# Optimization experiments

Hardware: AMD Instinct MI355X
Metric: run time of the kernel (lower is better)

## Reference

```python
import jax, jax.numpy as jnp
import numpy as np

HIDDEN = 2048
NUM_HEAD = 32
GROUP = 8
HEAD_DIM = HIDDEN // NUM_HEAD  # 64
REP = NUM_HEAD // GROUP        # 4


def setup_inputs() -> dict:
    key = jax.random.key(0)
    ks = jax.random.split(key, 9)
    s = 0.02
    kv_dim = GROUP * HEAD_DIM
    return {
        "hidden_states": jax.random.normal(ks[0], (2, 2048, HIDDEN), dtype=jnp.float32),
        "Wq": jax.random.normal(ks[1], (HIDDEN, HIDDEN), dtype=jnp.float32) * s,
        "bq": jnp.zeros((HIDDEN,), dtype=jnp.float32),
        "Wk": jax.random.normal(ks[2], (HIDDEN, kv_dim), dtype=jnp.float32) * s,
        "bk": jnp.zeros((kv_dim,), dtype=jnp.float32),
        "Wv": jax.random.normal(ks[3], (HIDDEN, kv_dim), dtype=jnp.float32) * s,
        "bv": jnp.zeros((kv_dim,), dtype=jnp.float32),
        "Wo": jax.random.normal(ks[4], (HIDDEN, HIDDEN), dtype=jnp.float32) * s,
        "bo": jnp.zeros((HIDDEN,), dtype=jnp.float32),
    }


def reference(hidden_states, Wq, bq, Wk, bk, Wv, bv, Wo, bo):
    B, S, H = hidden_states.shape
    q = hidden_states @ Wq + bq                      # [B,S,H]
    k = hidden_states @ Wk + bk                      # [B,S,G*hd]
    v = hidden_states @ Wv + bv
    q = q.reshape(B, S, NUM_HEAD, HEAD_DIM).transpose(0, 2, 1, 3)   # [B,nh,S,hd]
    k = k.reshape(B, S, GROUP, HEAD_DIM).transpose(0, 2, 1, 3)      # [B,G,S,hd]
    v = v.reshape(B, S, GROUP, HEAD_DIM).transpose(0, 2, 1, 3)
    # expand KV heads: each group head repeated REP times contiguously
    k = jnp.repeat(k, REP, axis=1)                   # [B,nh,S,hd]
    v = jnp.repeat(v, REP, axis=1)
    scale = 1.0 / jnp.sqrt(jnp.float32(HEAD_DIM))
    scores = jnp.einsum("bhqd,bhkd->bhqk", q, k) * scale  # [B,nh,S,S]
    attn = jax.nn.softmax(scores, axis=-1)
    out = jnp.einsum("bhqk,bhkd->bhqd", attn, v)     # [B,nh,S,hd]
    out = out.transpose(0, 2, 1, 3).reshape(B, S, NUM_HEAD * HEAD_DIM)
    return out @ Wo + bo
```

## Files before the change

kernel.cpp:

```cpp
#include <hip/hip_runtime.h>
#include <hip/hip_bf16.h>

typedef __attribute__((ext_vector_type(8))) short bf16x8;
typedef __attribute__((ext_vector_type(4))) short bf16x4;
typedef __attribute__((ext_vector_type(4))) float f32x4;

__device__ __forceinline__ unsigned short f2bf(float f) {
  union { float f; unsigned int u; } v; v.f = f;
  unsigned int r = (v.u + 0x7fffu + ((v.u >> 16) & 1u)) >> 16;
  return (unsigned short)r;
}

__device__ __forceinline__ unsigned int pk2bf(float a, float b) {
  float2 t; t.x = a; t.y = b;
  __hip_bfloat162 h = __float22bfloat162_rn(t);
  union { __hip_bfloat162 h; unsigned int u; } cv; cv.h = h;
  return cv.u;
}

__device__ __forceinline__ void g2l16(unsigned short* lds, const unsigned short* g) {
  __builtin_amdgcn_global_load_lds(
      (const __attribute__((address_space(1))) unsigned int*)g,
      (__attribute__((address_space(3))) unsigned int*)lds, 16, 0, 0);
}


__global__ __launch_bounds__(256) void cast_hs_kernel(const float* __restrict__ in,
                                                      unsigned short* __restrict__ out) {
  size_t i = (size_t)blockIdx.x * 256 + threadIdx.x;
  float4 v = ((const float4*)in)[i];
  ushort4 o;
  o.x = f2bf(v.x); o.y = f2bf(v.y); o.z = f2bf(v.z); o.w = f2bf(v.w);
  ((ushort4*)out)[i] = o;
}

__global__ __launch_bounds__(256) void transpose_all_kernel(
    const float* __restrict__ Wq, const float* __restrict__ Wk,
    const float* __restrict__ Wv, const float* __restrict__ Wo,
    unsigned short* __restrict__ Wqkv, unsigned short* __restrict__ WoT) {
  __shared__ float tile[32][33];
  int z = blockIdx.z;
  const float* src; unsigned short* dst; int N;
  if (z == 0)      { src = Wq; dst = Wqkv;                          N = 2048; }
  else if (z == 1) { src = Wk; dst = Wqkv + (size_t)2048 * 2048;    N = 512; }
  else if (z == 2) { src = Wv; dst = Wqkv + (size_t)2560 * 2048;    N = 512; }
  else             { src = Wo; dst = WoT;                           N = 2048; }
  if (blockIdx.x * 32 >= N) return;
  int n0 = blockIdx.x * 32, k0 = blockIdx.y * 32;
  int t = threadIdx.x;
  for (int i = 0; i < 4; ++i) {
    int linear = i * 256 + t;
    int kr = linear >> 5, nc = linear & 31;
    tile[kr][nc] = src[(size_t)(k0 + kr) * N + (n0 + nc)];
  }
  __syncthreads();
  for (int i = 0; i < 4; ++i) {
    int linear = i * 256 + t;
    int nr = linear >> 5, kc = linear & 31;
    dst[(size_t)(n0 + nr) * 2048 + (k0 + kc)] = f2bf(tile[kc][nr]);
  }
}


#define QSCALE 0.18033688011112042f

__global__ __launch_bounds__(256) void gemm_qkv_kernel(
    const unsigned short* __restrict__ A, const unsigned short* __restrict__ Bt,
    const float* __restrict__ bq, const float* __restrict__ bk, const float* __restrict__ bv,
    unsigned short* __restrict__ Qb, unsigned short* __restrict__ Kb,
    unsigned short* __restrict__ Vtb) {
  __shared__ __align__(16) unsigned short smem[128 * 136];
  unsigned short* sA = smem;
  unsigned short* sB = smem + 4096;
  const int K = 2048;
  int bm0 = blockIdx.y * 128, bn0 = blockIdx.x * 128;
  int t = threadIdx.x;
  int w = t >> 6, lane = t & 63, l16 = lane & 15, quad = lane >> 4;
  int wm = (w & 1) * 64, wn = (w >> 1) * 64;
  f32x4 zero = {0.f, 0.f, 0.f, 0.f};
  f32x4 acc[4][4];
  for (int mt = 0; mt < 4; ++mt)
    for (int nt = 0; nt < 4; ++nt) acc[mt][nt] = zero;

  for (int k0 = 0; k0 < K; k0 += 32) {
    for (int i = 0; i < 2; ++i) {
      int linear = i * 256 + t;
      int row = linear >> 2, kofs = (linear & 3) * 8;
      g2l16(sA + linear * 8, A + (size_t)(bm0 + row) * K + k0 + kofs);
      g2l16(sB + linear * 8, Bt + (size_t)(bn0 + row) * K + k0 + kofs);
    }
    __syncthreads();
    bf16x8 af[4], bfr[4];
    for (int mt = 0; mt < 4; ++mt)
      af[mt] = *(const bf16x8*)(sA + (wm + mt * 16 + l16) * 32 + quad * 8);
    for (int nt = 0; nt < 4; ++nt)
      bfr[nt] = *(const bf16x8*)(sB + (wn + nt * 16 + l16) * 32 + quad * 8);
    for (int mt = 0; mt < 4; ++mt)
      for (int nt = 0; nt < 4; ++nt)
        acc[mt][nt] = __builtin_amdgcn_mfma_f32_16x16x32_bf16(af[mt], bfr[nt], acc[mt][nt], 0, 0, 0);
    __syncthreads();
  }

  const int SP = 136;
  bool isV = (bn0 >= 2560);
  bool isQ = (bn0 < 2048);
  const float* bias = isQ ? bq : (bn0 < 2560 ? bk : bv);
  int nbase = isQ ? 0 : (bn0 < 2560 ? 2048 : 2560);

  for (int nt = 0; nt < 4; ++nt) {
    int nl = wn + nt * 16 + l16;
    float bb = bias[bn0 + nl - nbase];
    for (int mt = 0; mt < 4; ++mt)
      for (int r = 0; r < 4; ++r) {
        int ml = wm + mt * 16 + quad * 4 + r;
        float fv = acc[mt][nt][r] + bb;
        if (isQ) fv *= QSCALE;
        unsigned short val = f2bf(fv);
        if (isV) smem[nl * SP + ml] = val;
        else     smem[ml * SP + nl] = val;
      }
  }
  __syncthreads();

  int b = bm0 >> 11, s0 = bm0 & 2047;
  if (bn0 < 2048) {
    for (int i = 0; i < 8; ++i) {
      int idx = i * 256 + t;
      int sub = idx >> 10, s_l = (idx >> 3) & 127, dch = (idx & 7) * 8;
      bf16x8 v = *(const bf16x8*)(smem + s_l * SP + sub * 64 + dch);
      int n = bn0 + sub * 64 + dch;
      int h = n >> 6, d = n & 63;
      *(bf16x8*)(Qb + (((size_t)b * 32 + h) * 2048 + s0 + s_l) * 64 + d) = v;
    }
  } else if (bn0 < 2560) {
    for (int i = 0; i < 8; ++i) {
      int idx = i * 256 + t;
      int sub = idx >> 10, s_l = (idx >> 3) & 127, dch = (idx & 7) * 8;
      bf16x8 v = *(const bf16x8*)(smem + s_l * SP + sub * 64 + dch);
      int nn = bn0 + sub * 64 + dch - 2048;
      int g = nn >> 6, d = nn & 63;
      *(bf16x8*)(Kb + (((size_t)b * 8 + g) * 2048 + s0 + s_l) * 64 + d) = v;
    }
  } else {
    for (int i = 0; i < 8; ++i) {
      int idx = i * 256 + t;
      int nl = idx >> 4, sj = (idx & 15) * 8;
      bf16x8 v = *(const bf16x8*)(smem + nl * SP + sj);
      int nn = bn0 + nl - 2560;
      int g = nn >> 6, d = nn & 63;
      *(bf16x8*)(Vtb + (((size_t)b * 8 + g) * 64 + d) * 2048 + s0 + sj) = v;
    }
  }
}


__global__ __launch_bounds__(512, 8) void attn_kernel(
    const unsigned short* __restrict__ Qb, const unsigned short* __restrict__ Kb,
    const unsigned short* __restrict__ Vtb, unsigned short* __restrict__ AttnB) {
  __shared__ __align__(16) unsigned short Kt[64 * 64];
  __shared__ __align__(16) unsigned short Vt[64 * 64];
  int qt = blockIdx.x, h = blockIdx.y, b = blockIdx.z;
  int g = h >> 2;
  int t = threadIdx.x, w = t >> 6, lane = t & 63, l16 = lane & 15, quad = lane >> 4;

  const unsigned short* qb =
      Qb + (((size_t)b * 32 + h) * 2048 + qt * 128 + w * 16 + l16) * 64 + quad * 8;
  bf16x8 aQ0 = *(const bf16x8*)(qb);
  bf16x8 aQ1 = *(const bf16x8*)(qb + 32);

  const unsigned short* kbase = Kb + ((size_t)b * 8 + g) * (2048 * 64);
  const unsigned short* vbase = Vtb + ((size_t)b * 8 + g) * (64 * 2048);
  int r_ = t & 63, c_ = t >> 6;
  const unsigned short* gK = kbase + (size_t)r_ * 64 + c_ * 8;
  const unsigned short* gV = vbase + (size_t)r_ * 2048 + c_ * 8;
  unsigned short* wK = Kt + t * 8;
  unsigned short* wV = Vt + t * 8;

  f32x4 zero = {0.f, 0.f, 0.f, 0.f};
  f32x4 m10 = {-10.f, -10.f, -10.f, -10.f};
  union { unsigned short s[4]; bf16x4 v; } ones;
  ones.s[0] = 0x3F80; ones.s[1] = 0x3F80; ones.s[2] = 0x3F80; ones.s[3] = 0x3F80;

  f32x4 oA[4], olA;
  for (int dt = 0; dt < 4; ++dt) oA[dt] = zero;
  olA = zero;

  for (int kb = 0; kb < 32; ++kb) {
    g2l16(wK, gK + (size_t)kb * 4096);
    g2l16(wV, gV + (size_t)kb * 64);
    __syncthreads();

    for (int nt = 0; nt < 4; ++nt) {
      bf16x8 bk0 = *(const bf16x8*)(Kt + (quad * 64 + nt * 16 + l16) * 8);
      bf16x8 bk1 = *(const bf16x8*)(Kt + ((quad + 4) * 64 + nt * 16 + l16) * 8);
      f32x4 st = __builtin_amdgcn_mfma_f32_16x16x32_bf16(bk0, aQ0, m10, 0, 0, 0);
      st = __builtin_amdgcn_mfma_f32_16x16x32_bf16(bk1, aQ1, st, 0, 0, 0);

      union { unsigned int u[2]; bf16x4 v; } pa;
      pa.u[0] = pk2bf(__builtin_amdgcn_exp2f(st[0]), __builtin_amdgcn_exp2f(st[1]));
      pa.u[1] = pk2bf(__builtin_amdgcn_exp2f(st[2]), __builtin_amdgcn_exp2f(st[3]));

      olA = __builtin_amdgcn_mfma_f32_16x16x16bf16_1k(pa.v, ones.v, olA, 0, 0, 0);

      int c = nt * 2 + (quad >> 1);
      int ho = (quad & 1) * 4;
      for (int dt = 0; dt < 4; ++dt) {
        bf16x4 bv = *(const bf16x4*)(Vt + (c * 64 + dt * 16 + l16) * 8 + ho);
        oA[dt] = __builtin_amdgcn_mfma_f32_16x16x16bf16_1k(pa.v, bv, oA[dt], 0, 0, 0);
      }
    }
    __syncthreads();
  }

  for (int r = 0; r < 4; ++r) {
    float inv = 1.f / olA[r];
    int srow = qt * 128 + w * 16 + quad * 4 + r;
    size_t base = ((size_t)b * 2048 + srow) * 2048 + h * 64;
    for (int dt = 0; dt < 4; ++dt)
      AttnB[base + dt * 16 + l16] = f2bf(oA[dt][r] * inv);
  }
}


__global__ __launch_bounds__(256) void gemm_out_kernel(
    const unsigned short* __restrict__ A, const unsigned short* __restrict__ Bt,
    const float* __restrict__ bo, float* __restrict__ out) {
  __shared__ __align__(16) unsigned short sA[128 * 32];
  __shared__ __align__(16) unsigned short sB[128 * 32];
  const int K = 2048;
  int bm0 = blockIdx.y * 128, bn0 = blockIdx.x * 128;
  int t = threadIdx.x;
  int w = t >> 6, lane = t & 63, l16 = lane & 15, quad = lane >> 4;
  int wm = (w & 1) * 64, wn = (w >> 1) * 64;
  f32x4 zero = {0.f, 0.f, 0.f, 0.f};
  f32x4 acc[4][4];
  for (int mt = 0; mt < 4; ++mt)
    for (int nt = 0; nt < 4; ++nt) acc[mt][nt] = zero;

  for (int k0 = 0; k0 < K; k0 += 32) {
    for (int i = 0; i < 2; ++i) {
      int linear = i * 256 + t;
      int row = linear >> 2, kofs = (linear & 3) * 8;
      g2l16(sA + linear * 8, A + (size_t)(bm0 + row) * K + k0 + kofs);
      g2l16(sB + linear * 8, Bt + (size_t)(bn0 + row) * K + k0 + kofs);
    }
    __syncthreads();
    bf16x8 af[4], bfr[4];
    for (int mt = 0; mt < 4; ++mt)
      af[mt] = *(const bf16x8*)(sA + (wm + mt * 16 + l16) * 32 + quad * 8);
    for (int nt = 0; nt < 4; ++nt)
      bfr[nt] = *(const bf16x8*)(sB + (wn + nt * 16 + l16) * 32 + quad * 8);
    for (int mt = 0; mt < 4; ++mt)
      for (int nt = 0; nt < 4; ++nt)
        acc[mt][nt] = __builtin_amdgcn_mfma_f32_16x16x32_bf16(af[mt], bfr[nt], acc[mt][nt], 0, 0, 0);
    __syncthreads();
  }

  for (int nt = 0; nt < 4; ++nt) {
    int n = bn0 + wn + nt * 16 + l16;
    float bias = bo[n];
    for (int mt = 0; mt < 4; ++mt)
      for (int r = 0; r < 4; ++r) {
        int m = bm0 + wm + mt * 16 + quad * 4 + r;
        out[(size_t)m * 2048 + n] = acc[mt][nt][r] + bias;
      }
  }
}


extern "C" void kernel_launch(void* const* d_in, const int* in_sizes, int n_in,
                              void* d_out, int out_size, void* d_ws, size_t ws_size,
                              hipStream_t stream) {
  const float* hs = (const float*)d_in[0];
  const float* Wq = (const float*)d_in[1];
  const float* bq = (const float*)d_in[2];
  const float* Wk = (const float*)d_in[3];
  const float* bk = (const float*)d_in[4];
  const float* Wv = (const float*)d_in[5];
  const float* bv = (const float*)d_in[6];
  const float* Wo = (const float*)d_in[7];
  const float* bo = (const float*)d_in[8];
  float* out = (float*)d_out;

  char* ws = (char*)d_ws;
  unsigned short* hsb   = (unsigned short*)(ws);
  unsigned short* Wqkv  = (unsigned short*)(ws + 16777216);
  unsigned short* WoT   = (unsigned short*)(ws + 29360128);
  unsigned short* Qb    = (unsigned short*)(ws + 37748736);
  unsigned short* Kb    = (unsigned short*)(ws + 54525952);
  unsigned short* Vtb   = (unsigned short*)(ws + 58720256);
  unsigned short* AttnB = (unsigned short*)(ws + 62914560);

  hipLaunchKernelGGL(cast_hs_kernel, dim3(8192), dim3(256), 0, stream, hs, hsb);
  hipLaunchKernelGGL(transpose_all_kernel, dim3(64, 64, 4), dim3(256), 0, stream,
                     Wq, Wk, Wv, Wo, Wqkv, WoT);
  hipLaunchKernelGGL(gemm_qkv_kernel, dim3(24, 32), dim3(256), 0, stream,
                     hsb, Wqkv, bq, bk, bv, Qb, Kb, Vtb);
  hipLaunchKernelGGL(attn_kernel, dim3(16, 32, 2), dim3(512), 0, stream, Qb, Kb, Vtb, AttnB);
  hipLaunchKernelGGL(gemm_out_kernel, dim3(16, 32), dim3(256), 0, stream, AttnB, WoT, bo, out);
}
```

Baseline: 335.3 us.

## Double-buffer LDS tiles in QKV GEMM, attention and output GEMM loops

All three kernels now use two LDS buffers per operand. The next K tile (or K/V block) is prefetched with async global-to-LDS loads while MFMAs run on the current buffer, so each loop iteration needs one barrier instead of two. The aim is to hide global load latency behind compute. The cost is doubled shared memory per block, which matters most for the attention kernel and may reduce occupancy. The overlap may also be lost if the compiler inserts conservative vmcnt waits before the LDS reads.

```diff
diff --git a/kernel.cpp b/kernel.cpp
--- a/kernel.cpp
+++ b/kernel.cpp
@@ -70,8 +70,6 @@
     unsigned short* __restrict__ Qb, unsigned short* __restrict__ Kb,
     unsigned short* __restrict__ Vtb) {
   __shared__ __align__(16) unsigned short smem[128 * 136];
-  unsigned short* sA = smem;
-  unsigned short* sB = smem + 4096;
   const int K = 2048;
   int bm0 = blockIdx.y * 128, bn0 = blockIdx.x * 128;
   int t = threadIdx.x;
@@ -82,23 +80,34 @@
   for (int mt = 0; mt < 4; ++mt)
     for (int nt = 0; nt < 4; ++nt) acc[mt][nt] = zero;
 
-  for (int k0 = 0; k0 < K; k0 += 32) {
+  auto stage = [&](int buf, int k0) {
+    unsigned short* dA = smem + buf * 8192;
+    unsigned short* dB = dA + 4096;
     for (int i = 0; i < 2; ++i) {
       int linear = i * 256 + t;
       int row = linear >> 2, kofs = (linear & 3) * 8;
-      g2l16(sA + linear * 8, A + (size_t)(bm0 + row) * K + k0 + kofs);
-      g2l16(sB + linear * 8, Bt + (size_t)(bn0 + row) * K + k0 + kofs);
-    }
-    __syncthreads();
+      g2l16(dA + linear * 8, A + (size_t)(bm0 + row) * K + k0 + kofs);
+      g2l16(dB + linear * 8, Bt + (size_t)(bn0 + row) * K + k0 + kofs);
+    }
+  };
+
+  stage(0, 0);
+  __syncthreads();
+  int cur = 0;
+  for (int k0 = 0; k0 < K; k0 += 32) {
+    if (k0 + 32 < K) stage(cur ^ 1, k0 + 32);
+    const unsigned short* cA = smem + cur * 8192;
+    const unsigned short* cB = cA + 4096;
     bf16x8 af[4], bfr[4];
     for (int mt = 0; mt < 4; ++mt)
-      af[mt] = *(const bf16x8*)(sA + (wm + mt * 16 + l16) * 32 + quad * 8);
+      af[mt] = *(const bf16x8*)(cA + (wm + mt * 16 + l16) * 32 + quad * 8);
     for (int nt = 0; nt < 4; ++nt)
-      bfr[nt] = *(const bf16x8*)(sB + (wn + nt * 16 + l16) * 32 + quad * 8);
+      bfr[nt] = *(const bf16x8*)(cB + (wn + nt * 16 + l16) * 32 + quad * 8);
     for (int mt = 0; mt < 4; ++mt)
       for (int nt = 0; nt < 4; ++nt)
         acc[mt][nt] = __builtin_amdgcn_mfma_f32_16x16x32_bf16(af[mt], bfr[nt], acc[mt][nt], 0, 0, 0);
     __syncthreads();
+    cur ^= 1;
   }
 
   const int SP = 136;
@@ -157,8 +166,8 @@
 __global__ __launch_bounds__(512, 8) void attn_kernel(
     const unsigned short* __restrict__ Qb, const unsigned short* __restrict__ Kb,
     const unsigned short* __restrict__ Vtb, unsigned short* __restrict__ AttnB) {
-  __shared__ __align__(16) unsigned short Kt[64 * 64];
-  __shared__ __align__(16) unsigned short Vt[64 * 64];
+  __shared__ __align__(16) unsigned short Kt[2 * 4096];
+  __shared__ __align__(16) unsigned short Vt[2 * 4096];
   int qt = blockIdx.x, h = blockIdx.y, b = blockIdx.z;
   int g = h >> 2;
   int t = threadIdx.x, w = t >> 6, lane = t & 63, l16 = lane & 15, quad = lane >> 4;
@@ -173,8 +182,11 @@
   int r_ = t & 63, c_ = t >> 6;
   const unsigned short* gK = kbase + (size_t)r_ * 64 + c_ * 8;
   const unsigned short* gV = vbase + (size_t)r_ * 2048 + c_ * 8;
-  unsigned short* wK = Kt + t * 8;
-  unsigned short* wV = Vt + t * 8;
+
+  auto stage = [&](int buf, int kb) {
+    g2l16(Kt + buf * 4096 + t * 8, gK + (size_t)kb * 4096);
+    g2l16(Vt + buf * 4096 + t * 8, gV + (size_t)kb * 64);
+  };
 
   f32x4 zero = {0.f, 0.f, 0.f, 0.f};
   f32x4 m10 = {-10.f, -10.f, -10.f, -10.f};
@@ -185,14 +197,17 @@
   for (int dt = 0; dt < 4; ++dt) oA[dt] = zero;
   olA = zero;
 
+  stage(0, 0);
+  __syncthreads();
+  int cur = 0;
   for (int kb = 0; kb < 32; ++kb) {
-    g2l16(wK, gK + (size_t)kb * 4096);
-    g2l16(wV, gV + (size_t)kb * 64);
-    __syncthreads();
+    if (kb < 31) stage(cur ^ 1, kb + 1);
+    const unsigned short* Kc = Kt + cur * 4096;
+    const unsigned short* Vc = Vt + cur * 4096;
 
     for (int nt = 0; nt < 4; ++nt) {
-      bf16x8 bk0 = *(const bf16x8*)(Kt + (quad * 64 + nt * 16 + l16) * 8);
-      bf16x8 bk1 = *(const bf16x8*)(Kt + ((quad + 4) * 64 + nt * 16 + l16) * 8);
+      bf16x8 bk0 = *(const bf16x8*)(Kc + (quad * 64 + nt * 16 + l16) * 8);
+      bf16x8 bk1 = *(const bf16x8*)(Kc + ((quad + 4) * 64 + nt * 16 + l16) * 8);
       f32x4 st = __builtin_amdgcn_mfma_f32_16x16x32_bf16(bk0, aQ0, m10, 0, 0, 0);
       st = __builtin_amdgcn_mfma_f32_16x16x32_bf16(bk1, aQ1, st, 0, 0, 0);
 
@@ -205,11 +220,12 @@
       int c = nt * 2 + (quad >> 1);
       int ho = (quad & 1) * 4;
       for (int dt = 0; dt < 4; ++dt) {
-        bf16x4 bv = *(const bf16x4*)(Vt + (c * 64 + dt * 16 + l16) * 8 + ho);
+        bf16x4 bv = *(const bf16x4*)(Vc + (c * 64 + dt * 16 + l16) * 8 + ho);
         oA[dt] = __builtin_amdgcn_mfma_f32_16x16x16bf16_1k(pa.v, bv, oA[dt], 0, 0, 0);
       }
     }
     __syncthreads();
+    cur ^= 1;
   }
 
   for (int r = 0; r < 4; ++r) {
@@ -225,8 +241,7 @@
 __global__ __launch_bounds__(256) void gemm_out_kernel(
     const unsigned short* __restrict__ A, const unsigned short* __restrict__ Bt,
     const float* __restrict__ bo, float* __restrict__ out) {
-  __shared__ __align__(16) unsigned short sA[128 * 32];
-  __shared__ __align__(16) unsigned short sB[128 * 32];
+  __shared__ __align__(16) unsigned short smem[4 * 4096];
   const int K = 2048;
   int bm0 = blockIdx.y * 128, bn0 = blockIdx.x * 128;
   int t = threadIdx.x;
@@ -237,23 +252,34 @@
   for (int mt = 0; mt < 4; ++mt)
     for (int nt = 0; nt < 4; ++nt) acc[mt][nt] = zero;
 
-  for (int k0 = 0; k0 < K; k0 += 32) {
+  auto stage = [&](int buf, int k0) {
+    unsigned short* dA = smem + buf * 8192;
+    unsigned short* dB = dA + 4096;
     for (int i = 0; i < 2; ++i) {
       int linear = i * 256 + t;
       int row = linear >> 2, kofs = (linear & 3) * 8;
-      g2l16(sA + linear * 8, A + (size_t)(bm0 + row) * K + k0 + kofs);
-      g2l16(sB + linear * 8, Bt + (size_t)(bn0 + row) * K + k0 + kofs);
-    }
-    __syncthreads();
+      g2l16(dA + linear * 8, A + (size_t)(bm0 + row) * K + k0 + kofs);
+      g2l16(dB + linear * 8, Bt + (size_t)(bn0 + row) * K + k0 + kofs);
+    }
+  };
+
+  stage(0, 0);
+  __syncthreads();
+  int cur = 0;
+  for (int k0 = 0; k0 < K; k0 += 32) {
+    if (k0 + 32 < K) stage(cur ^ 1, k0 + 32);
+    const unsigned short* cA = smem + cur * 8192;
+    const unsigned short* cB = cA + 4096;
     bf16x8 af[4], bfr[4];
     for (int mt = 0; mt < 4; ++mt)
-      af[mt] = *(const bf16x8*)(sA + (wm + mt * 16 + l16) * 32 + quad * 8);
+      af[mt] = *(const bf16x8*)(cA + (wm + mt * 16 + l16) * 32 + quad * 8);
     for (int nt = 0; nt < 4; ++nt)
-      bfr[nt] = *(const bf16x8*)(sB + (wn + nt * 16 + l16) * 32 + quad * 8);
+      bfr[nt] = *(const bf16x8*)(cB + (wn + nt * 16 + l16) * 32 + quad * 8);
     for (int mt = 0; mt < 4; ++mt)
       for (int nt = 0; nt < 4; ++nt)
         acc[mt][nt] = __builtin_amdgcn_mfma_f32_16x16x32_bf16(af[mt], bfr[nt], acc[mt][nt], 0, 0, 0);
     __syncthreads();
+    cur ^= 1;
   }
 
   for (int nt = 0; nt < 4; ++nt) {
```

Result: slower. 344.9 us (+2.9%).
